# Kernel tuning notes

Measured on AMD Instinct MI355X. Metric: run time of the kernel, lower is better.

## Reference

```python
import jax, jax.numpy as jnp
import numpy as np

NUM_HEADS = 8
LN_EPS = 1e-5


def layer_norm(x, g, b):
    mu = jnp.mean(x, axis=-1, keepdims=True)
    var = jnp.var(x, axis=-1, keepdims=True)
    return (x - mu) * jax.lax.rsqrt(var + LN_EPS) * g + b


def mha(q, k, v, in_w, in_b, out_w, out_b):
    # torch nn.MultiheadAttention (batch_first): packed in_proj (3D,D), out_proj (D,D)
    B, Lq, D = q.shape
    Lk = k.shape[1]
    H = NUM_HEADS
    dh = D // H
    wq, wk, wv = in_w[:D], in_w[D:2 * D], in_w[2 * D:]
    bq, bk, bv = in_b[:D], in_b[D:2 * D], in_b[2 * D:]
    qp = (q @ wq.T + bq).reshape(B, Lq, H, dh).transpose(0, 2, 1, 3)
    kp = (k @ wk.T + bk).reshape(B, Lk, H, dh).transpose(0, 2, 1, 3)
    vp = (v @ wv.T + bv).reshape(B, Lk, H, dh).transpose(0, 2, 1, 3)
    scores = jnp.einsum('bhqd,bhkd->bhqk', qp, kp) / jnp.sqrt(jnp.asarray(dh, q.dtype))
    attn = jax.nn.softmax(scores, axis=-1)  # (B,H,Lq,Lk)
    out = jnp.einsum('bhqk,bhkd->bhqd', attn, vp)
    out = out.transpose(0, 2, 1, 3).reshape(B, Lq, D)
    return out @ out_w.T + out_b, attn


def setup_inputs() -> dict:
    key = jax.random.key(0)
    ks = jax.random.split(key, 8)
    B, P, Q, D = 32, 576, 256, 768
    s = 0.02
    return {
        'image_tokens': jax.random.normal(ks[0], (B, 1 + P, D), jnp.float32),
        'tactile_tokens': jax.random.normal(ks[1], (B, Q, D), jnp.float32),
        't2i_in_w': jax.random.normal(ks[2], (3 * D, D), jnp.float32) * s,
        't2i_in_b': jnp.zeros((3 * D,), jnp.float32),
        't2i_out_w': jax.random.normal(ks[3], (D, D), jnp.float32) * s,
        't2i_out_b': jnp.zeros((D,), jnp.float32),
        'i2t_in_w': jax.random.normal(ks[4], (3 * D, D), jnp.float32) * s,
        'i2t_in_b': jnp.zeros((3 * D,), jnp.float32),
        'i2t_out_w': jax.random.normal(ks[5], (D, D), jnp.float32) * s,
        'i2t_out_b': jnp.zeros((D,), jnp.float32),
        'ln_tact_g': jnp.ones((D,), jnp.float32),
        'ln_tact_b': jnp.zeros((D,), jnp.float32),
        'ln_img_g': jnp.ones((D,), jnp.float32),
        'ln_img_b': jnp.zeros((D,), jnp.float32),
    }


def reference(image_tokens, tactile_tokens, t2i_in_w, t2i_in_b, t2i_out_w, t2i_out_b,
              i2t_in_w, i2t_in_b, i2t_out_w, i2t_out_b,
              ln_tact_g, ln_tact_b, ln_img_g, ln_img_b):
    # attention_type == 'all_patch'
    cls_tok = image_tokens[:, :1, :]
    patch_tok = image_tokens[:, 1:, :]
    tact_out, attn_weights = mha(tactile_tokens, patch_tok, patch_tok,
                                 t2i_in_w, t2i_in_b, t2i_out_w, t2i_out_b)
    tactile_tokens = layer_norm(tactile_tokens + tact_out, ln_tact_g, ln_tact_b)
    patch_out, _ = mha(patch_tok, tactile_tokens, tactile_tokens,
                       i2t_in_w, i2t_in_b, i2t_out_w, i2t_out_b)
    patch_tok = layer_norm(patch_tok + patch_out, ln_img_g, ln_img_b)
    image_tokens = jnp.concatenate([cls_tok, patch_tok], axis=1)
    return image_tokens, tactile_tokens, attn_weights
```

## Files before the change

kernel.cpp:

```cpp
#include <hip/hip_runtime.h>
#include <stdint.h>
#include <math.h>

typedef unsigned short u16;
typedef __attribute__((ext_vector_type(8))) short bf16x8;
typedef __attribute__((ext_vector_type(4))) float f32x4;

__device__ __forceinline__ u16 f2b(float f) {
    unsigned u = __float_as_uint(f);
    u = (u + 0x7FFFu + ((u >> 16) & 1u)) >> 16;
    return (u16)u;
}

__device__ __forceinline__ void gload16(const void* g, void* lds) {
    __builtin_amdgcn_global_load_lds(
        (const __attribute__((address_space(1))) unsigned int*)(uintptr_t)g,
        (__attribute__((address_space(3))) unsigned int*)(unsigned int)(uintptr_t)lds,
        16, 0, 0);
}

#define BM 128
#define BN 128
#define BK 32

__global__ __launch_bounds__(256) void gemm_bt(
    const u16* __restrict__ A, const u16* __restrict__ B,
    const float* __restrict__ bias, const float* __restrict__ resid,
    float* __restrict__ Cf, u16* __restrict__ Cb,
    int M, int N, int K, int lda, int ldb, int ldc,
    float scale, int rgrp, long long rgA, long long rgoff, int ldr)
{
    __shared__ __align__(16) u16 lA[BM * BK];
    __shared__ __align__(16) u16 lB[BN * BK];

    const int tid = threadIdx.x;
    const int wave = tid >> 6;
    const int lane = tid & 63;

    const int tilesN = N / BN;
    const int tm = blockIdx.x / tilesN;
    const int tn = blockIdx.x % tilesN;
    const int row0 = tm * BM;
    const int col0 = tn * BN;

    const int f0 = tid * 8;
    const int f1 = (256 + tid) * 8;
    const int sr0 = f0 >> 5, sc0 = f0 & 31;
    const int sr1 = f1 >> 5, sc1 = f1 & 31;

    u16* lA0 = &lA[(wave * 64) * 8];
    u16* lA1 = &lA[2048 + (wave * 64) * 8];
    u16* lB0 = &lB[(wave * 64) * 8];
    u16* lB1 = &lB[2048 + (wave * 64) * 8];

    const u16* pa0 = A + (long long)(row0 + sr0) * lda + sc0;
    const u16* pa1 = A + (long long)(row0 + sr1) * lda + sc1;
    const u16* pb0 = B + (long long)(col0 + sr0) * ldb + sc0;
    const u16* pb1 = B + (long long)(col0 + sr1) * ldb + sc1;

    const int wr = wave >> 1, wc = wave & 1;
    const int fr = lane & 15;
    const int kk = (lane >> 4) * 8;

    f32x4 acc[4][4];
    #pragma unroll
    for (int m = 0; m < 4; ++m)
        #pragma unroll
        for (int n = 0; n < 4; ++n) {
            f32x4 z = {0.f, 0.f, 0.f, 0.f};
            acc[m][n] = z;
        }

    for (int k0 = 0; k0 < K; k0 += BK) {
        gload16(pa0 + k0, lA0);
        gload16(pa1 + k0, lA1);
        gload16(pb0 + k0, lB0);
        gload16(pb1 + k0, lB1);
        __syncthreads();

        bf16x8 af[4], bfv[4];
        #pragma unroll
        for (int m = 0; m < 4; ++m)
            af[m] = *(const bf16x8*)&lA[(wr * 64 + m * 16 + fr) * BK + kk];
        #pragma unroll
        for (int n = 0; n < 4; ++n)
            bfv[n] = *(const bf16x8*)&lB[(wc * 64 + n * 16 + fr) * BK + kk];
        #pragma unroll
        for (int m = 0; m < 4; ++m)
            #pragma unroll
            for (int n = 0; n < 4; ++n)
                acc[m][n] = __builtin_amdgcn_mfma_f32_16x16x32_bf16(af[m], bfv[n], acc[m][n], 0, 0, 0);
        __syncthreads();
    }

    const int orow = row0 + wr * 64;
    const int ocol = col0 + wc * 64;
    const int g4 = (lane >> 4) * 4;
    float bcol[4];
    #pragma unroll
    for (int n = 0; n < 4; ++n)
        bcol[n] = bias ? bias[ocol + n * 16 + fr] : 0.f;

    #pragma unroll
    for (int m = 0; m < 4; ++m) {
        #pragma unroll
        for (int j = 0; j < 4; ++j) {
            const int r = orow + m * 16 + g4 + j;
            long long ro = 0;
            if (resid) {
                unsigned q = (unsigned)r / (unsigned)rgrp;
                unsigned rem = (unsigned)r - q * (unsigned)rgrp;
                ro = (long long)q * rgA + (long long)rem * ldr + rgoff;
            }
            const long long crow = (long long)r * ldc;
            #pragma unroll
            for (int n = 0; n < 4; ++n) {
                const int c = ocol + n * 16 + fr;
                float v = acc[m][n][j] * scale + bcol[n];
                if (resid) v += resid[ro + c];
                if (Cb) Cb[crow + c] = f2b(v);
                else    Cf[crow + c] = v;
            }
        }
    }
}

template <bool WATTN>
__global__ __launch_bounds__(256, 2) void fused_attn(
    const u16* __restrict__ Q, const u16* __restrict__ K, const u16* __restrict__ Vt,
    float* __restrict__ attn, u16* __restrict__ O,
    int Lq, int Lk, int ldq, int ldk, int ldo)
{
    __shared__ __align__(16) u16 lQP[128 * 96];
    __shared__ __align__(16) u16 lKt[64 * 96];
    __shared__ __align__(16) u16 lVt[96 * 64];
    __shared__ float lM2[2][128], lL2[2][128];

    const int tid = threadIdx.x, wave = tid >> 6, lane = tid & 63;
    const int fr = lane & 15, g = lane >> 4;
    const int wr = wave >> 1, wc = wave & 1;
    const int z = blockIdx.y, b = z >> 3, h = z & 7;
    const int q0 = blockIdx.x * 128;
    const int nt = Lk >> 6;

    const u16* Qz = Q + (long long)b * Lq * ldq + h * 96;
    const u16* Kz = K + (long long)b * Lk * ldk + h * 96;
    const u16* Vz = Vt + (long long)z * 96 * Lk;
    u16* Oz = O + (long long)b * Lq * ldo + h * 96;
    float* Az = attn + (long long)z * Lq * Lk;

    const u16* qsrc[6];
    #pragma unroll
    for (int t = 0; t < 6; ++t) {
        int u = t * 256 + tid;
        int r = u / 12, cu = u % 12;
        int qr = q0 + r; if (qr > Lq - 1) qr = Lq - 1;
        qsrc[t] = Qz + (long long)qr * ldq + cu * 8;
    }
    const u16* ksrc[3];
    #pragma unroll
    for (int t = 0; t < 3; ++t) {
        int u = t * 256 + tid;
        int r = u / 12, cu = u % 12;
        ksrc[t] = Kz + (long long)r * ldk + cu * 8;
    }
    const u16* vsrc[3];
    #pragma unroll
    for (int t = 0; t < 3; ++t) {
        int u = t * 256 + tid;
        int d = u >> 3, uu = u & 7;
        vsrc[t] = Vz + (long long)d * Lk + ((uu ^ (d & 7)) * 8);
    }
    const long long kstep = 64LL * ldk;

    #define DQ(t) ((char*)lQP + ((t) * 256 + wave * 64) * 16)
    #define DK(t) ((char*)lKt + ((t) * 256 + wave * 64) * 16)
    #define DV(t) ((char*)lVt + ((t) * 256 + wave * 64) * 16)

    #pragma unroll
    for (int t = 0; t < 6; ++t) gload16(qsrc[t], DQ(t));
    #pragma unroll
    for (int t = 0; t < 3; ++t) gload16(ksrc[t], DK(t));
    __syncthreads();

    bf16x8 qf[4][3];
    #pragma unroll
    for (int m = 0; m < 4; ++m)
        #pragma unroll
        for (int ks = 0; ks < 3; ++ks)
            qf[m][ks] = *(const bf16x8*)((const char*)lQP + (wr * 64 + m * 16 + fr) * 192 + ks * 64 + g * 16);

    float m_run[4], l_run[4];
    #pragma unroll
    for (int i = 0; i < 4; ++i) { m_run[i] = -1e30f; l_run[i] = 0.f; }

    for (int i = 0; i < nt; ++i) {
        bf16x8 kf[2][3];
        #pragma unroll
        for (int mk = 0; mk < 2; ++mk)
            #pragma unroll
            for (int ks = 0; ks < 3; ++ks)
                kf[mk][ks] = *(const bf16x8*)((const char*)lKt + (wc * 32 + mk * 16 + fr) * 192 + ks * 64 + g * 16);
        f32x4 sa[2][4];
        #pragma unroll
        for (int mk = 0; mk < 2; ++mk)
            #pragma unroll
            for (int nq = 0; nq < 4; ++nq) {
                f32x4 zz = {0.f, 0.f, 0.f, 0.f};
                sa[mk][nq] = zz;
            }
        #pragma unroll
        for (int ks = 0; ks < 3; ++ks)
            #pragma unroll
            for (int mk = 0; mk < 2; ++mk)
                #pragma unroll
                for (int nq = 0; nq < 4; ++nq)
                    sa[mk][nq] = __builtin_amdgcn_mfma_f32_16x16x32_bf16(kf[mk][ks], qf[nq][ks], sa[mk][nq], 0, 0, 0);
        #pragma unroll
        for (int nq = 0; nq < 4; ++nq) {
            float tmx = -1e30f;
            #pragma unroll
            for (int mk = 0; mk < 2; ++mk)
                #pragma unroll
                for (int j = 0; j < 4; ++j)
                    tmx = fmaxf(tmx, sa[mk][nq][j]);
            tmx = fmaxf(tmx, __shfl_xor(tmx, 16));
            tmx = fmaxf(tmx, __shfl_xor(tmx, 32));
            const float mnew = fmaxf(m_run[nq], tmx);
            float ts = 0.f;
            #pragma unroll
            for (int mk = 0; mk < 2; ++mk)
                #pragma unroll
                for (int j = 0; j < 4; ++j)
                    ts += __expf(sa[mk][nq][j] - mnew);
            ts += __shfl_xor(ts, 16);
            ts += __shfl_xor(ts, 32);
            l_run[nq] = l_run[nq] * __expf(m_run[nq] - mnew) + ts;
            m_run[nq] = mnew;
        }
        __syncthreads();
        if (i + 1 < nt) {
            #pragma unroll
            for (int t = 0; t < 3; ++t) { ksrc[t] += kstep; gload16(ksrc[t], DK(t)); }
        }
        __syncthreads();
    }

    if (g == 0) {
        #pragma unroll
        for (int nq = 0; nq < 4; ++nq) {
            lM2[wc][wr * 64 + nq * 16 + fr] = m_run[nq];
            lL2[wc][wr * 64 + nq * 16 + fr] = l_run[nq];
        }
    }
    #pragma unroll
    for (int t = 0; t < 3; ++t) ksrc[t] -= (long long)(nt - 1) * kstep;
    #pragma unroll
    for (int t = 0; t < 3; ++t) gload16(ksrc[t], DK(t));
    #pragma unroll
    for (int t = 0; t < 3; ++t) gload16(vsrc[t], DV(t));
    __syncthreads();

    float mrow[16], linv[16];
    #pragma unroll
    for (int m = 0; m < 4; ++m)
        #pragma unroll
        for (int j = 0; j < 4; ++j) {
            const int q = wr * 64 + m * 16 + g * 4 + j;
            const float ma = lM2[0][q], mb = lM2[1][q];
            const float mm = fmaxf(ma, mb);
            const float ll = lL2[0][q] * __expf(ma - mm) + lL2[1][q] * __expf(mb - mm);
            mrow[m * 4 + j] = mm;
            linv[m * 4 + j] = 1.f / ll;
        }

    f32x4 oacc[4][3];
    #pragma unroll
    for (int m = 0; m < 4; ++m)
        #pragma unroll
        for (int nd = 0; nd < 3; ++nd) {
            f32x4 zz = {0.f, 0.f, 0.f, 0.f};
            oacc[m][nd] = zz;
        }

    for (int i = 0; i < nt; ++i) {
        const int k0 = i * 64;
        bf16x8 kf[2][3];
        #pragma unroll
        for (int n = 0; n < 2; ++n)
            #pragma unroll
            for (int ks = 0; ks < 3; ++ks)
                kf[n][ks] = *(const bf16x8*)((const char*)lKt + (wc * 32 + n * 16 + fr) * 192 + ks * 64 + g * 16);
        f32x4 ss[4][2];
        #pragma unroll
        for (int m = 0; m < 4; ++m)
            #pragma unroll
            for (int n = 0; n < 2; ++n) {
                f32x4 zz = {0.f, 0.f, 0.f, 0.f};
                ss[m][n] = zz;
            }
        #pragma unroll
        for (int ks = 0; ks < 3; ++ks)
            #pragma unroll
            for (int m = 0; m < 4; ++m)
                #pragma unroll
                for (int n = 0; n < 2; ++n)
                    ss[m][n] = __builtin_amdgcn_mfma_f32_16x16x32_bf16(qf[m][ks], kf[n][ks], ss[m][n], 0, 0, 0);
        __syncthreads();
        if (i + 1 < nt) {
            #pragma unroll
            for (int t = 0; t < 3; ++t) { ksrc[t] += kstep; gload16(ksrc[t], DK(t)); }
        }
        #pragma unroll
        for (int m = 0; m < 4; ++m)
            #pragma unroll
            for (int n = 0; n < 2; ++n)
                #pragma unroll
                for (int j = 0; j < 4; ++j) {
                    const float p = __expf(ss[m][n][j] - mrow[m * 4 + j]) * linv[m * 4 + j];
                    const int q = wr * 64 + m * 16 + g * 4 + j;
                    const int k = wc * 32 + n * 16 + fr;
                    if (WATTN) Az[(long long)(q0 + q) * Lk + k0 + k] = p;
                    *(u16*)((char*)lQP + q * 144 + k * 2) = f2b(p);
                }
        __syncthreads();
        #pragma unroll
        for (int ks = 0; ks < 2; ++ks) {
            bf16x8 vf[3], pf[4];
            #pragma unroll
            for (int nd = 0; nd < 3; ++nd) {
                const int row = wc * 48 + nd * 16 + fr;
                vf[nd] = *(const bf16x8*)((const char*)lVt + row * 128 + (((ks * 4 + g) ^ (row & 7)) * 16));
            }
            #pragma unroll
            for (int m = 0; m < 4; ++m)
                pf[m] = *(const bf16x8*)((const char*)lQP + (wr * 64 + m * 16 + fr) * 144 + ks * 64 + g * 16);
            #pragma unroll
            for (int m = 0; m < 4; ++m)
                #pragma unroll
                for (int nd = 0; nd < 3; ++nd)
                    oacc[m][nd] = __builtin_amdgcn_mfma_f32_16x16x32_bf16(pf[m], vf[nd], oacc[m][nd], 0, 0, 0);
        }
        __syncthreads();
        if (i + 1 < nt) {
            #pragma unroll
            for (int t = 0; t < 3; ++t) { vsrc[t] += 64; gload16(vsrc[t], DV(t)); }
        }
    }

    #pragma unroll
    for (int m = 0; m < 4; ++m)
        #pragma unroll
        for (int j = 0; j < 4; ++j) {
            const int q = q0 + wr * 64 + m * 16 + g * 4 + j;
            if (q < Lq) {
                #pragma unroll
                for (int nd = 0; nd < 3; ++nd) {
                    const int c = wc * 48 + nd * 16 + fr;
                    Oz[(long long)q * ldo + c] = f2b(oacc[m][nd][j]);
                }
            }
        }
    #undef DQ
    #undef DK
    #undef DV
}

__global__ __launch_bounds__(256) void transpose_v(
    const u16* __restrict__ V, u16* __restrict__ Vt, int L, int ldv)
{
    __shared__ unsigned int t[64 * 97];
    const int z = blockIdx.y;
    const int b = z >> 3, h = z & 7;
    const int l0 = blockIdx.x * 64;
    const int tid = threadIdx.x;
    for (int i = 0; i < 24; ++i) {
        const int idx = tid + i * 256;
        const int l = idx / 96, d = idx % 96;
        t[l * 97 + d] = V[((long long)(b * L + l0 + l)) * ldv + h * 96 + d];
    }
    __syncthreads();
    for (int i = 0; i < 24; ++i) {
        const int idx = tid + i * 256;
        const int d = idx / 64, l = idx % 64;
        Vt[((long long)z * 96 + d) * L + l0 + l] = (u16)t[l * 97 + d];
    }
}

__global__ __launch_bounds__(256) void ln_k(
    const float* __restrict__ X, const float* __restrict__ g, const float* __restrict__ b,
    float* __restrict__ outF, u16* __restrict__ outB,
    int rows, int grp, long long gA, long long goff, int ldo)
{
    const int wave = threadIdx.x >> 6, lane = threadIdx.x & 63;
    const int row = blockIdx.x * 4 + wave;
    if (row >= rows) return;
    const float* x = X + (long long)row * 768;
    float v[12], s = 0.f, sq = 0.f;
    #pragma unroll
    for (int i = 0; i < 12; ++i) { v[i] = x[lane + 64 * i]; s += v[i]; sq += v[i] * v[i]; }
    #pragma unroll
    for (int o = 32; o; o >>= 1) { s += __shfl_xor(s, o); sq += __shfl_xor(sq, o); }
    const float mu = s * (1.f / 768.f);
    const float var = sq * (1.f / 768.f) - mu * mu;
    const float inv = rsqrtf(var + 1e-5f);
    const long long ob = (long long)(row / grp) * gA + (long long)(row % grp) * ldo + goff;
    #pragma unroll
    for (int i = 0; i < 12; ++i) {
        const int c = lane + 64 * i;
        const float y = (v[i] - mu) * inv * g[c] + b[c];
        outF[ob + c] = y;
        if (outB) outB[(long long)row * 768 + c] = f2b(y);
    }
}

__global__ __launch_bounds__(256) void conv_f2b(
    const float4* __restrict__ in, u16* __restrict__ out, long long n4)
{
    long long i = (long long)blockIdx.x * 256 + threadIdx.x;
    const long long stride = (long long)gridDim.x * 256;
    for (; i < n4; i += stride) {
        const float4 f = in[i];
        ushort4 u;
        u.x = f2b(f.x); u.y = f2b(f.y); u.z = f2b(f.z); u.w = f2b(f.w);
        ((ushort4*)out)[i] = u;
    }
}

__global__ __launch_bounds__(256) void conv_patch(
    const float* __restrict__ img, u16* __restrict__ out)
{
    long long i = (long long)blockIdx.x * 256 + threadIdx.x;
    const long long n4 = 18432LL * 192;
    const long long stride = (long long)gridDim.x * 256;
    for (; i < n4; i += stride) {
        const long long r = i / 192; const int c4 = (int)(i % 192);
        const long long sr = (r / 576) * 577 + 1 + (r % 576);
        const float4 f = ((const float4*)img)[sr * 192 + c4];
        ushort4 u;
        u.x = f2b(f.x); u.y = f2b(f.y); u.z = f2b(f.z); u.w = f2b(f.w);
        ((ushort4*)out)[i] = u;
    }
}

__global__ __launch_bounds__(256) void cls_copy(
    const float* __restrict__ img, float* __restrict__ out)
{
    const int i = blockIdx.x * 256 + threadIdx.x;
    if (i < 32 * 768) {
        const int b = i / 768, c = i % 768;
        out[(long long)b * 577 * 768 + c] = img[(long long)b * 577 * 768 + c];
    }
}

static inline void launch_gemm(hipStream_t s,
    const u16* A, const u16* Bm, const float* bias, const float* resid,
    float* Cf, u16* Cb, int M, int N, int K, int lda, int ldb, int ldc,
    float scale, int rgrp, long long rgA, long long rgoff, int ldr)
{
    dim3 grid((unsigned)((M / BM) * (N / BN)));
    gemm_bt<<<grid, dim3(256), 0, s>>>(A, Bm, bias, resid, Cf, Cb,
        M, N, K, lda, ldb, ldc, scale, rgrp, rgA, rgoff, ldr);
}

extern "C" void kernel_launch(void* const* d_in, const int* in_sizes, int n_in,
                              void* d_out, int out_size, void* d_ws, size_t ws_size,
                              hipStream_t stream)
{
    (void)in_sizes; (void)n_in; (void)out_size; (void)ws_size;
    const float* img   = (const float*)d_in[0];
    const float* tac   = (const float*)d_in[1];
    const float* w1in  = (const float*)d_in[2];
    const float* b1in  = (const float*)d_in[3];
    const float* w1out = (const float*)d_in[4];
    const float* b1out = (const float*)d_in[5];
    const float* w2in  = (const float*)d_in[6];
    const float* b2in  = (const float*)d_in[7];
    const float* w2out = (const float*)d_in[8];
    const float* b2out = (const float*)d_in[9];
    const float* lng1  = (const float*)d_in[10];
    const float* lnb1  = (const float*)d_in[11];
    const float* lng2  = (const float*)d_in[12];
    const float* lnb2  = (const float*)d_in[13];
    float* out = (float*)d_out;

    const long long o_tac  = 32LL * 577 * 768;
    const long long o_attn = o_tac + 32LL * 256 * 768;
    const float qscale = 1.0f / sqrtf(96.0f);

    char* ws = (char*)d_ws;
    u16* tact_bf    = (u16*)ws;
    u16* patch_bf   = tact_bf + 8192LL * 768;
    u16* w1in_bf    = patch_bf + 18432LL * 768;
    u16* w1out_bf   = w1in_bf + 2304LL * 768;
    u16* w2in_bf    = w1out_bf + 768LL * 768;
    u16* w2out_bf   = w2in_bf + 2304LL * 768;
    u16* tactnew_bf = w2out_bf + 768LL * 768;
    char* sbase     = (char*)(tactnew_bf + 8192LL * 768);

    u16* Q1  = (u16*)sbase;
    u16* KV1 = Q1 + 8192LL * 768;
    u16* Vt1 = KV1 + 18432LL * 1536;
    u16* AO1 = Vt1 + 256LL * 96 * 576;
    float* O1s = (float*)Vt1;
    u16* Q2  = (u16*)sbase;
    u16* KV2 = Q2 + 18432LL * 768;
    u16* Vt2 = KV2 + 8192LL * 1536;
    u16* AO2 = Vt2 + 256LL * 96 * 256;
    float* O2s = (float*)sbase;

    conv_f2b<<<1024, 256, 0, stream>>>((const float4*)tac, tact_bf, 8192LL * 192);
    conv_patch<<<1024, 256, 0, stream>>>(img, patch_bf);
    conv_f2b<<<512, 256, 0, stream>>>((const float4*)w1in, w1in_bf, 2304LL * 192);
    conv_f2b<<<512, 256, 0, stream>>>((const float4*)w1out, w1out_bf, 768LL * 192);
    conv_f2b<<<512, 256, 0, stream>>>((const float4*)w2in, w2in_bf, 2304LL * 192);
    conv_f2b<<<512, 256, 0, stream>>>((const float4*)w2out, w2out_bf, 768LL * 192);
    cls_copy<<<96, 256, 0, stream>>>(img, out);

    launch_gemm(stream, tact_bf, w1in_bf, b1in, nullptr, nullptr, Q1,
        8192, 768, 768, 768, 768, 768, qscale, 1, 0, 0, 0);
    launch_gemm(stream, patch_bf, w1in_bf + 768LL * 768, b1in + 768, nullptr, nullptr, KV1,
        18432, 1536, 768, 768, 768, 1536, 1.0f, 1, 0, 0, 0);
    transpose_v<<<dim3(9, 256), 256, 0, stream>>>(KV1 + 768, Vt1, 576, 1536);
    fused_attn<true><<<dim3(2, 256), 256, 0, stream>>>(
        Q1, KV1, Vt1, out + o_attn, AO1, 256, 576, 768, 1536, 768);
    launch_gemm(stream, AO1, w1out_bf, b1out, tac, O1s, nullptr,
        8192, 768, 768, 768, 768, 768, 1.0f, 1, 768, 0, 0);
    ln_k<<<8192 / 4, 256, 0, stream>>>(O1s, lng1, lnb1, out + o_tac, tactnew_bf,
        8192, 8192, 0, 0, 768);

    launch_gemm(stream, patch_bf, w2in_bf, b2in, nullptr, nullptr, Q2,
        18432, 768, 768, 768, 768, 768, qscale, 1, 0, 0, 0);
    launch_gemm(stream, tactnew_bf, w2in_bf + 768LL * 768, b2in + 768, nullptr, nullptr, KV2,
        8192, 1536, 768, 768, 768, 1536, 1.0f, 1, 0, 0, 0);
    transpose_v<<<dim3(4, 256), 256, 0, stream>>>(KV2 + 768, Vt2, 256, 1536);
    fused_attn<false><<<dim3(5, 256), 256, 0, stream>>>(
        Q2, KV2, Vt2, nullptr, AO2, 576, 256, 768, 1536, 768);
    launch_gemm(stream, AO2, w2out_bf, b2out, img, O2s, nullptr,
        18432, 768, 768, 768, 768, 768, 1.0f, 576, 577LL * 768, 768, 768);
    ln_k<<<18432 / 4, 256, 0, stream>>>(O2s, lng2, lnb2, out, nullptr,
        18432, 576, 577LL * 768, 768, 768);
}
```

Baseline: 836.2 us.

## Group independent projection GEMMs, double-buffer LDS tiles, merge weight conversions

Replaces the single-GEMM kernel with a grouped GEMM that runs up to three independent problems in one launch. The Q1, KV1 and Q2 projections, which all depend only on the inputs, now share one launch. The K loop now double-buffers the LDS tiles so the next tile's global-to-LDS load is issued before the current tile's MFMAs, which removes one barrier per iteration. It also interleaves the block-to-tile mapping across 8 groups, fuses the four weight conversions into a single kernel, and gives every buffer its own workspace region instead of aliasing, which uses more workspace memory.

```diff
diff --git a/kernel.cpp b/kernel.cpp
--- a/kernel.cpp
+++ b/kernel.cpp
@@ -23,23 +23,36 @@
 #define BN 128
 #define BK 32
 
-__global__ __launch_bounds__(256) void gemm_bt(
-    const u16* __restrict__ A, const u16* __restrict__ B,
-    const float* __restrict__ bias, const float* __restrict__ resid,
-    float* __restrict__ Cf, u16* __restrict__ Cb,
-    int M, int N, int K, int lda, int ldb, int ldc,
-    float scale, int rgrp, long long rgA, long long rgoff, int ldr)
-{
-    __shared__ __align__(16) u16 lA[BM * BK];
-    __shared__ __align__(16) u16 lB[BN * BK];
+struct GemmGrp {
+    const u16* A; const u16* B; const float* bias; const float* resid;
+    float* Cf; u16* Cb;
+    int M, N, lda, ldb, ldc;
+    float scale;
+    int rgrp; long long rgA, rgoff; int ldr;
+};
+struct G3 { GemmGrp g[3]; int start[4]; int K; };
+
+__global__ __launch_bounds__(256) void gemm_grp(G3 P)
+{
+    __shared__ __align__(16) u16 lA[2][BM * BK];
+    __shared__ __align__(16) u16 lB[2][BN * BK];
 
     const int tid = threadIdx.x;
     const int wave = tid >> 6;
     const int lane = tid & 63;
 
-    const int tilesN = N / BN;
-    const int tm = blockIdx.x / tilesN;
-    const int tn = blockIdx.x % tilesN;
+    const int ntot = P.start[3];
+    int L = blockIdx.x;
+    if ((ntot & 7) == 0) L = (L & 7) * (ntot >> 3) + (L >> 3);
+
+    const int gi = (L >= P.start[1]) + (L >= P.start[2]);
+    GemmGrp g;
+    if (gi == 0) g = P.g[0]; else if (gi == 1) g = P.g[1]; else g = P.g[2];
+    const int t = L - P.start[gi];
+
+    const int tilesN = g.N / BN;
+    const int tm = t / tilesN;
+    const int tn = t % tilesN;
     const int row0 = tm * BM;
     const int col0 = tn * BN;
 
@@ -48,15 +61,10 @@
     const int sr0 = f0 >> 5, sc0 = f0 & 31;
     const int sr1 = f1 >> 5, sc1 = f1 & 31;
 
-    u16* lA0 = &lA[(wave * 64) * 8];
-    u16* lA1 = &lA[2048 + (wave * 64) * 8];
-    u16* lB0 = &lB[(wave * 64) * 8];
-    u16* lB1 = &lB[2048 + (wave * 64) * 8];
-
-    const u16* pa0 = A + (long long)(row0 + sr0) * lda + sc0;
-    const u16* pa1 = A + (long long)(row0 + sr1) * lda + sc1;
-    const u16* pb0 = B + (long long)(col0 + sr0) * ldb + sc0;
-    const u16* pb1 = B + (long long)(col0 + sr1) * ldb + sc1;
+    const u16* pa0 = g.A + (long long)(row0 + sr0) * g.lda + sc0;
+    const u16* pa1 = g.A + (long long)(row0 + sr1) * g.lda + sc1;
+    const u16* pb0 = g.B + (long long)(col0 + sr0) * g.ldb + sc0;
+    const u16* pb1 = g.B + (long long)(col0 + sr1) * g.ldb + sc1;
 
     const int wr = wave >> 1, wc = wave & 1;
     const int fr = lane & 15;
@@ -71,27 +79,34 @@
             acc[m][n] = z;
         }
 
-    for (int k0 = 0; k0 < K; k0 += BK) {
-        gload16(pa0 + k0, lA0);
-        gload16(pa1 + k0, lA1);
-        gload16(pb0 + k0, lB0);
-        gload16(pb1 + k0, lB1);
-        __syncthreads();
-
+    #define STAGE(buf, k0) do { \
+        gload16(pa0 + (k0), &lA[buf][(wave * 64) * 8]); \
+        gload16(pa1 + (k0), &lA[buf][2048 + (wave * 64) * 8]); \
+        gload16(pb0 + (k0), &lB[buf][(wave * 64) * 8]); \
+        gload16(pb1 + (k0), &lB[buf][2048 + (wave * 64) * 8]); \
+    } while (0)
+
+    STAGE(0, 0);
+    __syncthreads();
+    int cur = 0;
+    for (int k0 = 0; k0 < P.K; k0 += BK) {
+        if (k0 + BK < P.K) STAGE(cur ^ 1, k0 + BK);
         bf16x8 af[4], bfv[4];
         #pragma unroll
         for (int m = 0; m < 4; ++m)
-            af[m] = *(const bf16x8*)&lA[(wr * 64 + m * 16 + fr) * BK + kk];
+            af[m] = *(const bf16x8*)&lA[cur][(wr * 64 + m * 16 + fr) * BK + kk];
         #pragma unroll
         for (int n = 0; n < 4; ++n)
-            bfv[n] = *(const bf16x8*)&lB[(wc * 64 + n * 16 + fr) * BK + kk];
+            bfv[n] = *(const bf16x8*)&lB[cur][(wc * 64 + n * 16 + fr) * BK + kk];
         #pragma unroll
         for (int m = 0; m < 4; ++m)
             #pragma unroll
             for (int n = 0; n < 4; ++n)
                 acc[m][n] = __builtin_amdgcn_mfma_f32_16x16x32_bf16(af[m], bfv[n], acc[m][n], 0, 0, 0);
         __syncthreads();
-    }
+        cur ^= 1;
+    }
+    #undef STAGE
 
     const int orow = row0 + wr * 64;
     const int ocol = col0 + wc * 64;
@@ -99,7 +114,7 @@
     float bcol[4];
     #pragma unroll
     for (int n = 0; n < 4; ++n)
-        bcol[n] = bias ? bias[ocol + n * 16 + fr] : 0.f;
+        bcol[n] = g.bias ? g.bias[ocol + n * 16 + fr] : 0.f;
 
     #pragma unroll
     for (int m = 0; m < 4; ++m) {
@@ -107,19 +122,19 @@
         for (int j = 0; j < 4; ++j) {
             const int r = orow + m * 16 + g4 + j;
             long long ro = 0;
-            if (resid) {
-                unsigned q = (unsigned)r / (unsigned)rgrp;
-                unsigned rem = (unsigned)r - q * (unsigned)rgrp;
-                ro = (long long)q * rgA + (long long)rem * ldr + rgoff;
+            if (g.resid) {
+                unsigned q = (unsigned)r / (unsigned)g.rgrp;
+                unsigned rem = (unsigned)r - q * (unsigned)g.rgrp;
+                ro = (long long)q * g.rgA + (long long)rem * g.ldr + g.rgoff;
             }
-            const long long crow = (long long)r * ldc;
+            const long long crow = (long long)r * g.ldc;
             #pragma unroll
             for (int n = 0; n < 4; ++n) {
                 const int c = ocol + n * 16 + fr;
-                float v = acc[m][n][j] * scale + bcol[n];
-                if (resid) v += resid[ro + c];
-                if (Cb) Cb[crow + c] = f2b(v);
-                else    Cf[crow + c] = v;
+                float v = acc[m][n][j] * g.scale + bcol[n];
+                if (g.resid) v += g.resid[ro + c];
+                if (g.Cb) g.Cb[crow + c] = f2b(v);
+                else      g.Cf[crow + c] = v;
             }
         }
     }
@@ -427,6 +442,28 @@
     }
 }
 
+__global__ __launch_bounds__(256) void conv_w4(
+    const float4* __restrict__ a, const float4* __restrict__ b,
+    const float4* __restrict__ c, const float4* __restrict__ d,
+    u16* __restrict__ oa, u16* __restrict__ ob,
+    u16* __restrict__ oc, u16* __restrict__ od)
+{
+    const long long n1 = 442368, n2 = 589824, n3 = 1032192, n4 = 1179648;
+    long long i = (long long)blockIdx.x * 256 + threadIdx.x;
+    const long long stride = (long long)gridDim.x * 256;
+    for (; i < n4; i += stride) {
+        const float4* src; u16* dst; long long k;
+        if (i < n1)      { src = a; dst = oa; k = i; }
+        else if (i < n2) { src = b; dst = ob; k = i - n1; }
+        else if (i < n3) { src = c; dst = oc; k = i - n2; }
+        else             { src = d; dst = od; k = i - n3; }
+        const float4 f = src[k];
+        ushort4 u;
+        u.x = f2b(f.x); u.y = f2b(f.y); u.z = f2b(f.z); u.w = f2b(f.w);
+        ((ushort4*)dst)[k] = u;
+    }
+}
+
 __global__ __launch_bounds__(256) void conv_patch(
     const float* __restrict__ img, u16* __restrict__ out)
 {
@@ -453,14 +490,29 @@
     }
 }
 
-static inline void launch_gemm(hipStream_t s,
-    const u16* A, const u16* Bm, const float* bias, const float* resid,
-    float* Cf, u16* Cb, int M, int N, int K, int lda, int ldb, int ldc,
-    float scale, int rgrp, long long rgA, long long rgoff, int ldr)
-{
-    dim3 grid((unsigned)((M / BM) * (N / BN)));
-    gemm_bt<<<grid, dim3(256), 0, s>>>(A, Bm, bias, resid, Cf, Cb,
-        M, N, K, lda, ldb, ldc, scale, rgrp, rgA, rgoff, ldr);
+static inline GemmGrp mkgrp(const u16* A, const u16* B, const float* bias,
+    const float* resid, float* Cf, u16* Cb, int M, int N, int lda, int ldb,
+    int ldc, float scale, int rgrp, long long rgA, long long rgoff, int ldr)
+{
+    GemmGrp g;
+    g.A = A; g.B = B; g.bias = bias; g.resid = resid; g.Cf = Cf; g.Cb = Cb;
+    g.M = M; g.N = N; g.lda = lda; g.ldb = ldb; g.ldc = ldc;
+    g.scale = scale; g.rgrp = rgrp; g.rgA = rgA; g.rgoff = rgoff; g.ldr = ldr;
+    return g;
+}
+
+static inline void launch_grp(hipStream_t s, const GemmGrp* gs, int ng, int K)
+{
+    G3 P;
+    P.start[0] = 0;
+    for (int i = 0; i < 3; ++i) {
+        const GemmGrp& src = gs[i < ng ? i : ng - 1];
+        P.g[i] = src;
+        const int nb = (i < ng) ? (src.M / BM) * (src.N / BN) : 0;
+        P.start[i + 1] = P.start[i] + nb;
+    }
+    P.K = K;
+    gemm_grp<<<dim3((unsigned)P.start[3]), dim3(256), 0, s>>>(P);
 }
 
 extern "C" void kernel_launch(void* const* d_in, const int* in_sizes, int n_in,
@@ -488,56 +540,68 @@
     const long long o_attn = o_tac + 32LL * 256 * 768;
     const float qscale = 1.0f / sqrtf(96.0f);
 
-    char* ws = (char*)d_ws;
-    u16* tact_bf    = (u16*)ws;
-    u16* patch_bf   = tact_bf + 8192LL * 768;
-    u16* w1in_bf    = patch_bf + 18432LL * 768;
-    u16* w1out_bf   = w1in_bf + 2304LL * 768;
-    u16* w2in_bf    = w1out_bf + 768LL * 768;
-    u16* w2out_bf   = w2in_bf + 2304LL * 768;
-    u16* tactnew_bf = w2out_bf + 768LL * 768;
-    char* sbase     = (char*)(tactnew_bf + 8192LL * 768);
-
-    u16* Q1  = (u16*)sbase;
-    u16* KV1 = Q1 + 8192LL * 768;
-    u16* Vt1 = KV1 + 18432LL * 1536;
-    u16* AO1 = Vt1 + 256LL * 96 * 576;
-    float* O1s = (float*)Vt1;
-    u16* Q2  = (u16*)sbase;
-    u16* KV2 = Q2 + 18432LL * 768;
-    u16* Vt2 = KV2 + 8192LL * 1536;
-    u16* AO2 = Vt2 + 256LL * 96 * 256;
-    float* O2s = (float*)sbase;
+    u16* p = (u16*)d_ws;
+    u16* tact_bf    = p; p += 8192LL * 768;
+    u16* patch_bf   = p; p += 18432LL * 768;
+    u16* w1in_bf    = p; p += 2304LL * 768;
+    u16* w1out_bf   = p; p += 768LL * 768;
+    u16* w2in_bf    = p; p += 2304LL * 768;
+    u16* w2out_bf   = p; p += 768LL * 768;
+    u16* tactnew_bf = p; p += 8192LL * 768;
+    u16* Q1  = p; p += 8192LL * 768;
+    u16* KV1 = p; p += 18432LL * 1536;
+    u16* Vt1 = p; p += 256LL * 96 * 576;
+    u16* AO1 = p; p += 8192LL * 768;
+    u16* Q2  = p; p += 18432LL * 768;
+    u16* KV2 = p; p += 8192LL * 1536;
+    u16* Vt2 = p; p += 256LL * 96 * 256;
+    u16* AO2 = p; p += 18432LL * 768;
+    float* O1s = (float*)p; p += 2LL * 8192 * 768;
+    float* O2s = (float*)p; p += 2LL * 18432 * 768;
 
     conv_f2b<<<1024, 256, 0, stream>>>((const float4*)tac, tact_bf, 8192LL * 192);
     conv_patch<<<1024, 256, 0, stream>>>(img, patch_bf);
-    conv_f2b<<<512, 256, 0, stream>>>((const float4*)w1in, w1in_bf, 2304LL * 192);
-    conv_f2b<<<512, 256, 0, stream>>>((const float4*)w1out, w1out_bf, 768LL * 192);
-    conv_f2b<<<512, 256, 0, stream>>>((const float4*)w2in, w2in_bf, 2304LL * 192);
-    conv_f2b<<<512, 256, 0, stream>>>((const float4*)w2out, w2out_bf, 768LL * 192);
+    conv_w4<<<1024, 256, 0, stream>>>(
+        (const float4*)w1in, (const float4*)w1out, (const float4*)w2in, (const float4*)w2out,
+        w1in_bf, w1out_bf, w2in_bf, w2out_bf);
     cls_copy<<<96, 256, 0, stream>>>(img, out);
 
-    launch_gemm(stream, tact_bf, w1in_bf, b1in, nullptr, nullptr, Q1,
-        8192, 768, 768, 768, 768, 768, qscale, 1, 0, 0, 0);
-    launch_gemm(stream, patch_bf, w1in_bf + 768LL * 768, b1in + 768, nullptr, nullptr, KV1,
-        18432, 1536, 768, 768, 768, 1536, 1.0f, 1, 0, 0, 0);
+    {
+        GemmGrp gs[3] = {
+            mkgrp(tact_bf,  w1in_bf,              b1in,       nullptr, nullptr, Q1,
+                  8192, 768, 768, 768, 768, qscale, 1, 0, 0, 0),
+            mkgrp(patch_bf, w1in_bf + 768LL*768,  b1in + 768, nullptr, nullptr, KV1,
+                  18432, 1536, 768, 768, 1536, 1.0f, 1, 0, 0, 0),
+            mkgrp(patch_bf, w2in_bf,              b2in,       nullptr, nullptr, Q2,
+                  18432, 768, 768, 768, 768, qscale, 1, 0, 0, 0)
+        };
+        launch_grp(stream, gs, 3, 768);
+    }
+
     transpose_v<<<dim3(9, 256), 256, 0, stream>>>(KV1 + 768, Vt1, 576, 1536);
     fused_attn<true><<<dim3(2, 256), 256, 0, stream>>>(
         Q1, KV1, Vt1, out + o_attn, AO1, 256, 576, 768, 1536, 768);
-    launch_gemm(stream, AO1, w1out_bf, b1out, tac, O1s, nullptr,
-        8192, 768, 768, 768, 768, 768, 1.0f, 1, 768, 0, 0);
+    {
+        GemmGrp g = mkgrp(AO1, w1out_bf, b1out, tac, O1s, nullptr,
+                          8192, 768, 768, 768, 768, 1.0f, 1, 768, 0, 0);
+        launch_grp(stream, &g, 1, 768);
+    }
     ln_k<<<8192 / 4, 256, 0, stream>>>(O1s, lng1, lnb1, out + o_tac, tactnew_bf,
         8192, 8192, 0, 0, 768);
 
-    launch_gemm(stream, patch_bf, w2in_bf, b2in, nullptr, nullptr, Q2,
-        18432, 768, 768, 768, 768, 768, qscale, 1, 0, 0, 0);
-    launch_gemm(stream, tactnew_bf, w2in_bf + 768LL * 768, b2in + 768, nullptr, nullptr, KV2,
-        8192, 1536, 768, 768, 768, 1536, 1.0f, 1, 0, 0, 0);
+    {
+        GemmGrp g = mkgrp(tactnew_bf, w2in_bf + 768LL*768, b2in + 768, nullptr,
+                          nullptr, KV2, 8192, 1536, 768, 768, 1536, 1.0f, 1, 0, 0, 0);
+        launch_grp(stream, &g, 1, 768);
+    }
     transpose_v<<<dim3(4, 256), 256, 0, stream>>>(KV2 + 768, Vt2, 256, 1536);
     fused_attn<false><<<dim3(5, 256), 256, 0, stream>>>(
         Q2, KV2, Vt2, nullptr, AO2, 576, 256, 768, 1536, 768);
-    launch_gemm(stream, AO2, w2out_bf, b2out, img, O2s, nullptr,
-        18432, 768, 768, 768, 768, 768, 1.0f, 576, 577LL * 768, 768, 768);
+    {
+        GemmGrp g = mkgrp(AO2, w2out_bf, b2out, img, O2s, nullptr,
+                          18432, 768, 768, 768, 768, 1.0f, 576, 577LL * 768, 768, 768);
+        launch_grp(stream, &g, 1, 768);
+    }
     ln_k<<<18432 / 4, 256, 0, stream>>>(O2s, lng2, lnb2, out, nullptr,
         18432, 576, 577LL * 768, 768, 768);
 }
```

Result: faster. 764.8 us (-8.5%).
